# Kernel optimization log

Measured on AMD Instinct MI355X. Metric: run time of the kernel, lower is better.

The kernel has to match this reference:

```python
import jax, jax.numpy as jnp
import numpy as np

B, S, D_IN, D_OUT = 4, 2048, 1024, 1024

def setup_inputs() -> dict:
    key = jax.random.key(0)
    k1, k2, k3, k4 = jax.random.split(key, 4)
    x = jax.random.normal(k1, (B, S, D_IN), dtype=jnp.float32)
    # nn.Linear weights: [out, in]; y = x @ W.T
    scale = 1.0 / np.sqrt(D_IN)
    W_key = jax.random.uniform(k2, (D_OUT, D_IN), dtype=jnp.float32, minval=-scale, maxval=scale)
    W_query = jax.random.uniform(k3, (D_OUT, D_IN), dtype=jnp.float32, minval=-scale, maxval=scale)
    W_value = jax.random.uniform(k4, (D_OUT, D_IN), dtype=jnp.float32, minval=-scale, maxval=scale)
    return {"x": x, "W_key": W_key, "W_query": W_query, "W_value": W_value}

def reference(x, W_key, W_query, W_value):
    # x: [B, S, D_IN]; W_*: [D_OUT, D_IN]
    keys = jnp.einsum('bsd,od->bso', x, W_key)
    queries = jnp.einsum('bsd,od->bso', x, W_query)
    values = jnp.einsum('bsd,od->bso', x, W_value)
    # attn_scores: [B, S, S]
    scores = jnp.einsum('bqo,bko->bqk', queries, keys)
    inv_sqrt_d = 1.0 / jnp.sqrt(jnp.asarray(keys.shape[-1], dtype=scores.dtype))
    weights = jax.nn.softmax(scores * inv_sqrt_d, axis=-1)
    context = jnp.einsum('bqk,bko->bqo', weights, values)
    return context
```

## Files before the change

### kernel.cpp

```cpp
#include <hip/hip_runtime.h>

typedef unsigned short u16;
typedef __attribute__((ext_vector_type(4))) float f32x4;
typedef __attribute__((ext_vector_type(8))) short bf16x8;
typedef __attribute__((ext_vector_type(4))) u16 u16x4;
typedef __attribute__((ext_vector_type(8))) u16 u16x8;

__device__ __forceinline__ u16 f2bf(float f) {
    unsigned u = __float_as_uint(f);
    unsigned r = (u + 0x7FFFu + ((u >> 16) & 1u)) >> 16;
    return (u16)r;
}

__device__ __forceinline__ void gld16(const void* g, void* l) {
    __builtin_amdgcn_global_load_lds(
        (const __attribute__((address_space(1))) unsigned*)g,
        (__attribute__((address_space(3))) unsigned*)l,
        16, 0, 0);
}

__device__ __forceinline__ void xcd_map(int& bx, int& by, int& bz) {
    const int gx = gridDim.x, gxy = gridDim.x * gridDim.y;
    const int F = blockIdx.x + gx * (blockIdx.y + gridDim.y * blockIdx.z);
    const int cpx = (gxy * gridDim.z) >> 3;
    const int L = (F & 7) * cpx + (F >> 3);
    bz = L / gxy;
    const int r = L % gxy;
    by = r / gx;
    bx = r % gx;
}

__global__ __launch_bounds__(256) void prep_kernel(
    const float* __restrict__ x, const float* __restrict__ Wq,
    const float* __restrict__ Wk, const float* __restrict__ Wv,
    u16* __restrict__ xb, u16* __restrict__ wqk, u16* __restrict__ wvb,
    float* __restrict__ den) {
    const int NX = 2097152, NW = 262144;
    const int total = NX + 3 * NW + 2048;
    int i = blockIdx.x * blockDim.x + threadIdx.x;
    int stride = gridDim.x * blockDim.x;
    for (; i < total; i += stride) {
        const float* src; u16* dst; int j;
        if (i < NX)               { src = x;  dst = xb;            j = i; }
        else if (i < NX + NW)     { src = Wq; dst = wqk;           j = i - NX; }
        else if (i < NX + 2 * NW) { src = Wk; dst = wqk + 1048576; j = i - NX - NW; }
        else if (i < NX + 3 * NW) { src = Wv; dst = wvb;           j = i - NX - 2 * NW; }
        else { ((f32x4*)den)[i - NX - 3 * NW] = f32x4{0.f, 0.f, 0.f, 0.f}; continue; }
        f32x4 v = ((const f32x4*)src)[j];
        u16x4 o;
        o[0] = f2bf(v[0]); o[1] = f2bf(v[1]); o[2] = f2bf(v[2]); o[3] = f2bf(v[3]);
        ((u16x4*)dst)[j] = o;
    }
}

template <int EPI>
__global__ __launch_bounds__(512, 1) void gemm256(
    const u16* __restrict__ A, const u16* __restrict__ Bm, void* __restrict__ Cv,
    int K, int lda, int ldb, int ldc,
    long long sA, long long sB, long long sC, float scale,
    float* __restrict__ denom) {
    extern __shared__ char smem[];
    int bx, by, bz;
    xcd_map(bx, by, bz);
    const u16* Ab = A + (long long)bz * sA;
    const u16* Bb = Bm + (long long)bz * sB;

    const int tid  = threadIdx.x;
    const int lane = tid & 63;
    const int w    = tid >> 6;
    const int wm   = w >> 2;
    const int wn   = w & 3;
    const int rowBase = bx << 8;
    const int colBase = by << 8;
    const int NT = K >> 6;
    const int aRow = lane & 15;

    auto stage = [&](int tile, int h) {
        if (tile >= NT) return;
        const int db = tile & 1;
        const int kt = tile << 6;
        const u16* mat; int ldm, rb, halfRow; char* region;
        if (h == 0)      { mat = Ab; ldm = lda; rb = rowBase; halfRow = 0;   region = smem + db * 32768; }
        else if (h == 1) { mat = Bb; ldm = ldb; rb = colBase; halfRow = 0;   region = smem + 65536 + db * 32768; }
        else if (h == 2) { mat = Bb; ldm = ldb; rb = colBase; halfRow = 128; region = smem + 65536 + db * 32768; }
        else             { mat = Ab; ldm = lda; rb = rowBase; halfRow = 128; region = smem + db * 32768; }
#pragma unroll
        for (int i = 0; i < 2; i++) {
            int o    = ((i * 8 + w) << 10) + lane * 16;
            int r    = o >> 7;
            int slot = (o >> 4) & 7;
            const u16* g = mat + (size_t)(rb + halfRow + r) * ldm + kt +
                           ((slot ^ (r & 7)) << 3);
            gld16(g, region + halfRow * 128 + ((i * 8 + w) << 10));
        }
    };
    auto ldA = [&](int db, int row, int ks) -> bf16x8 {
        int byte = db * 32768 + row * 128 + ((((ks << 2) | (lane >> 4)) ^ (row & 7)) << 4);
        return *(const bf16x8*)(smem + byte);
    };
    auto ldB = [&](int db, int row, int ks) -> bf16x8 {
        int byte = 65536 + db * 32768 + row * 128 + ((((ks << 2) | (lane >> 4)) ^ (row & 7)) << 4);
        return *(const bf16x8*)(smem + byte);
    };

    f32x4 acc[8][4] = {};
    bf16x8 aF[4][2], b0[2][2], b1[2][2];

    stage(0, 0); stage(0, 3); stage(0, 1); stage(0, 2);
    stage(1, 1); stage(1, 2);
    __builtin_amdgcn_sched_barrier(0);
    asm volatile("s_waitcnt vmcnt(4)" ::: "memory");
    __builtin_amdgcn_sched_barrier(0);
    __builtin_amdgcn_s_barrier();

    for (int t = 0; t < NT; ++t) {
        const int db = t & 1;
#pragma unroll
        for (int m = 0; m < 4; m++)
#pragma unroll
            for (int ks = 0; ks < 2; ks++)
                aF[m][ks] = ldA(db, wm * 128 + m * 16 + aRow, ks);
#pragma unroll
        for (int n = 0; n < 2; n++)
#pragma unroll
            for (int ks = 0; ks < 2; ks++)
                b0[n][ks] = ldB(db, wn * 64 + n * 16 + aRow, ks);
        stage(t + 1, 0);
        __builtin_amdgcn_s_barrier();
        asm volatile("s_waitcnt lgkmcnt(0)" ::: "memory");
        __builtin_amdgcn_sched_barrier(0);
        __builtin_amdgcn_s_setprio(1);
#pragma unroll
        for (int ks = 0; ks < 2; ks++)
#pragma unroll
            for (int m = 0; m < 4; m++)
#pragma unroll
                for (int n = 0; n < 2; n++)
                    acc[m][n] = __builtin_amdgcn_mfma_f32_16x16x32_bf16(
                        aF[m][ks], b0[n][ks], acc[m][n], 0, 0, 0);
        __builtin_amdgcn_s_setprio(0);
#pragma unroll
        for (int n = 0; n < 2; n++)
#pragma unroll
            for (int ks = 0; ks < 2; ks++)
                b1[n][ks] = ldB(db, wn * 64 + (n + 2) * 16 + aRow, ks);
        stage(t + 1, 3);
        __builtin_amdgcn_s_barrier();
        asm volatile("s_waitcnt lgkmcnt(0)" ::: "memory");
        __builtin_amdgcn_sched_barrier(0);
        __builtin_amdgcn_s_setprio(1);
#pragma unroll
        for (int ks = 0; ks < 2; ks++)
#pragma unroll
            for (int m = 0; m < 4; m++)
#pragma unroll
                for (int n = 0; n < 2; n++)
                    acc[m][n + 2] = __builtin_amdgcn_mfma_f32_16x16x32_bf16(
                        aF[m][ks], b1[n][ks], acc[m][n + 2], 0, 0, 0);
        __builtin_amdgcn_s_setprio(0);
#pragma unroll
        for (int m = 0; m < 4; m++)
#pragma unroll
            for (int ks = 0; ks < 2; ks++)
                aF[m][ks] = ldA(db, wm * 128 + (m + 4) * 16 + aRow, ks);
        __builtin_amdgcn_s_barrier();
        asm volatile("s_waitcnt lgkmcnt(0)" ::: "memory");
        __builtin_amdgcn_sched_barrier(0);
        __builtin_amdgcn_s_setprio(1);
#pragma unroll
        for (int ks = 0; ks < 2; ks++)
#pragma unroll
            for (int m = 0; m < 4; m++)
#pragma unroll
                for (int n = 0; n < 2; n++)
                    acc[m + 4][n + 2] = __builtin_amdgcn_mfma_f32_16x16x32_bf16(
                        aF[m][ks], b1[n][ks], acc[m + 4][n + 2], 0, 0, 0);
        __builtin_amdgcn_s_setprio(0);
        stage(t + 2, 1);
        stage(t + 2, 2);
        __builtin_amdgcn_sched_barrier(0);
        if (t + 2 < NT) { asm volatile("s_waitcnt vmcnt(4)" ::: "memory"); }
        else            { asm volatile("s_waitcnt vmcnt(0)" ::: "memory"); }
        __builtin_amdgcn_sched_barrier(0);
        __builtin_amdgcn_s_barrier();
        __builtin_amdgcn_s_setprio(1);
#pragma unroll
        for (int ks = 0; ks < 2; ks++)
#pragma unroll
            for (int m = 0; m < 4; m++)
#pragma unroll
                for (int n = 0; n < 2; n++)
                    acc[m + 4][n] = __builtin_amdgcn_mfma_f32_16x16x32_bf16(
                        aF[m][ks], b0[n][ks], acc[m + 4][n], 0, 0, 0);
        __builtin_amdgcn_s_setprio(0);
    }

    const int row0 = rowBase + wm * 128 + ((lane >> 4) << 2);
    const int col0 = colBase + wn * 64 + (lane & 15);
    long long cb = (long long)bz * sC;
    if (EPI == 0) {
#pragma unroll
        for (int m = 0; m < 8; m++)
#pragma unroll
            for (int n = 0; n < 4; n++) {
                f32x4 v = acc[m][n];
#pragma unroll
                for (int j = 0; j < 4; j++) {
                    size_t idx = (size_t)(row0 + m * 16 + j) * ldc + (col0 + n * 16);
                    ((u16*)Cv)[cb + idx] = f2bf(v[j] * scale);
                }
            }
    } else {
        float* dz = denom + (long long)bz * 2048;
#pragma unroll
        for (int m = 0; m < 8; m++) {
#pragma unroll
            for (int j = 0; j < 4; j++) {
                const int row = row0 + m * 16 + j;
                float rs = 0.f;
#pragma unroll
                for (int n = 0; n < 4; n++) {
                    float e = __expf(fminf(acc[m][n][j] * scale, 60.f));
                    rs += e;
                    ((u16*)Cv)[cb + (size_t)row * ldc + (col0 + n * 16)] = f2bf(e);
                }
#pragma unroll
                for (int off = 1; off < 16; off <<= 1) rs += __shfl_xor(rs, off);
                if ((lane & 15) == 0) atomicAdd(&dz[row], rs);
            }
        }
    }
}

template <int EPI>
__global__ __launch_bounds__(512, 1) void gemm256n128(
    const u16* __restrict__ A, const u16* __restrict__ Bm, void* __restrict__ Cv,
    int K, int lda, int ldb, int ldc,
    long long sA, long long sB, long long sC, float scale,
    const float* __restrict__ denom) {
    extern __shared__ char smem[];
    int bx, by, bz;
    xcd_map(bx, by, bz);
    const u16* Ab = A + (long long)bz * sA;
    const u16* Bb = Bm + (long long)bz * sB;

    const int tid  = threadIdx.x;
    const int lane = tid & 63;
    const int w    = tid >> 6;
    const int wm   = w >> 1;
    const int wn   = w & 1;
    const int rowBase = bx << 8;
    const int colBase = by << 7;
    const int NT = K >> 6;
    const int aRow = lane & 15;

    auto stage = [&](int tile, int h) {
        if (tile >= NT) return;
        const int db = tile & 1;
        const int kt = tile << 6;
        if (h == 0 || h == 3) {
            const int halfRow = (h == 0) ? 0 : 128;
            char* region = smem + db * 32768;
#pragma unroll
            for (int i = 0; i < 2; i++) {
                int o    = i * 8192 + tid * 16;
                int r    = o >> 7;
                int slot = (o >> 4) & 7;
                const u16* g = Ab + (size_t)(rowBase + halfRow + r) * lda + kt +
                               ((slot ^ (r & 7)) << 3);
                gld16(g, region + halfRow * 128 + i * 8192 + (w << 10));
            }
        } else {
            const int halfRow = (h == 1) ? 0 : 64;
            char* region = smem + 65536 + db * 16384;
            int o    = tid * 16;
            int r    = o >> 7;
            int slot = (o >> 4) & 7;
            const u16* g = Bb + (size_t)(colBase + halfRow + r) * ldb + kt +
                           ((slot ^ (r & 7)) << 3);
            gld16(g, region + halfRow * 128 + (w << 10));
        }
    };
    auto ldA = [&](int db, int row, int ks) -> bf16x8 {
        int byte = db * 32768 + row * 128 + ((((ks << 2) | (lane >> 4)) ^ (row & 7)) << 4);
        return *(const bf16x8*)(smem + byte);
    };
    auto ldB = [&](int db, int row, int ks) -> bf16x8 {
        int byte = 65536 + db * 16384 + row * 128 + ((((ks << 2) | (lane >> 4)) ^ (row & 7)) << 4);
        return *(const bf16x8*)(smem + byte);
    };

    f32x4 acc[4][4] = {};
    bf16x8 aF[2][2], b0[2][2], b1[2][2];

    stage(0, 0); stage(0, 3); stage(0, 1); stage(0, 2);
    stage(1, 1); stage(1, 2);
    __builtin_amdgcn_sched_barrier(0);
    asm volatile("s_waitcnt vmcnt(2)" ::: "memory");
    __builtin_amdgcn_sched_barrier(0);
    __builtin_amdgcn_s_barrier();

    for (int t = 0; t < NT; ++t) {
        const int db = t & 1;
#pragma unroll
        for (int m = 0; m < 2; m++)
#pragma unroll
            for (int ks = 0; ks < 2; ks++)
                aF[m][ks] = ldA(db, wm * 64 + m * 16 + aRow, ks);
#pragma unroll
        for (int n = 0; n < 2; n++)
#pragma unroll
            for (int ks = 0; ks < 2; ks++)
                b0[n][ks] = ldB(db, wn * 64 + n * 16 + aRow, ks);
        stage(t + 1, 0);
        __builtin_amdgcn_s_barrier();
        asm volatile("s_waitcnt lgkmcnt(0)" ::: "memory");
        __builtin_amdgcn_sched_barrier(0);
        __builtin_amdgcn_s_setprio(1);
#pragma unroll
        for (int ks = 0; ks < 2; ks++)
#pragma unroll
            for (int m = 0; m < 2; m++)
#pragma unroll
                for (int n = 0; n < 2; n++)
                    acc[m][n] = __builtin_amdgcn_mfma_f32_16x16x32_bf16(
                        aF[m][ks], b0[n][ks], acc[m][n], 0, 0, 0);
        __builtin_amdgcn_s_setprio(0);
#pragma unroll
        for (int n = 0; n < 2; n++)
#pragma unroll
            for (int ks = 0; ks < 2; ks++)
                b1[n][ks] = ldB(db, wn * 64 + (n + 2) * 16 + aRow, ks);
        stage(t + 1, 3);
        __builtin_amdgcn_s_barrier();
        asm volatile("s_waitcnt lgkmcnt(0)" ::: "memory");
        __builtin_amdgcn_sched_barrier(0);
        __builtin_amdgcn_s_setprio(1);
#pragma unroll
        for (int ks = 0; ks < 2; ks++)
#pragma unroll
            for (int m = 0; m < 2; m++)
#pragma unroll
                for (int n = 0; n < 2; n++)
                    acc[m][n + 2] = __builtin_amdgcn_mfma_f32_16x16x32_bf16(
                        aF[m][ks], b1[n][ks], acc[m][n + 2], 0, 0, 0);
        __builtin_amdgcn_s_setprio(0);
#pragma unroll
        for (int m = 0; m < 2; m++)
#pragma unroll
            for (int ks = 0; ks < 2; ks++)
                aF[m][ks] = ldA(db, wm * 64 + (m + 2) * 16 + aRow, ks);
        __builtin_amdgcn_s_barrier();
        asm volatile("s_waitcnt lgkmcnt(0)" ::: "memory");
        __builtin_amdgcn_sched_barrier(0);
        __builtin_amdgcn_s_setprio(1);
#pragma unroll
        for (int ks = 0; ks < 2; ks++)
#pragma unroll
            for (int m = 0; m < 2; m++)
#pragma unroll
                for (int n = 0; n < 2; n++)
                    acc[m + 2][n + 2] = __builtin_amdgcn_mfma_f32_16x16x32_bf16(
                        aF[m][ks], b1[n][ks], acc[m + 2][n + 2], 0, 0, 0);
        __builtin_amdgcn_s_setprio(0);
        stage(t + 2, 1);
        stage(t + 2, 2);
        __builtin_amdgcn_sched_barrier(0);
        if (t + 2 < NT) { asm volatile("s_waitcnt vmcnt(2)" ::: "memory"); }
        else            { asm volatile("s_waitcnt vmcnt(0)" ::: "memory"); }
        __builtin_amdgcn_sched_barrier(0);
        __builtin_amdgcn_s_barrier();
        __builtin_amdgcn_s_setprio(1);
#pragma unroll
        for (int ks = 0; ks < 2; ks++)
#pragma unroll
            for (int m = 0; m < 2; m++)
#pragma unroll
                for (int n = 0; n < 2; n++)
                    acc[m + 2][n] = __builtin_amdgcn_mfma_f32_16x16x32_bf16(
                        aF[m][ks], b0[n][ks], acc[m + 2][n], 0, 0, 0);
        __builtin_amdgcn_s_setprio(0);
    }

    const int row0 = rowBase + wm * 64 + ((lane >> 4) << 2);
    const int col0 = colBase + wn * 64 + (lane & 15);
    long long cb = (long long)bz * sC;
    if (EPI == 0) {
#pragma unroll
        for (int m = 0; m < 4; m++)
#pragma unroll
            for (int n = 0; n < 4; n++) {
                f32x4 v = acc[m][n];
#pragma unroll
                for (int j = 0; j < 4; j++) {
                    size_t idx = (size_t)(row0 + m * 16 + j) * ldc + (col0 + n * 16);
                    ((u16*)Cv)[cb + idx] = f2bf(v[j] * scale);
                }
            }
    } else {
        const float* dz = denom + (long long)bz * 2048;
        float inv[4][4];
#pragma unroll
        for (int m = 0; m < 4; m++)
#pragma unroll
            for (int j = 0; j < 4; j++)
                inv[m][j] = 1.0f / dz[row0 + m * 16 + j];
#pragma unroll
        for (int m = 0; m < 4; m++)
#pragma unroll
            for (int n = 0; n < 4; n++) {
                f32x4 v = acc[m][n];
#pragma unroll
                for (int j = 0; j < 4; j++) {
                    size_t idx = (size_t)(row0 + m * 16 + j) * ldc + (col0 + n * 16);
                    ((float*)Cv)[cb + idx] = v[j] * inv[m][j];
                }
            }
    }
}

extern "C" void kernel_launch(void* const* d_in, const int* in_sizes, int n_in,
                              void* d_out, int out_size, void* d_ws, size_t ws_size,
                              hipStream_t stream) {
    const float* x  = (const float*)d_in[0];
    const float* Wk = (const float*)d_in[1];
    const float* Wq = (const float*)d_in[2];
    const float* Wv = (const float*)d_in[3];
    float* out = (float*)d_out;
    char* ws = (char*)d_ws;
    const size_t MB = 1u << 20;

    u16* xb    = (u16*)(ws);
    u16* Wqk   = (u16*)(ws + 16 * MB);
    u16* Wvb   = (u16*)(ws + 20 * MB);
    float* den = (float*)(ws + 24 * MB);
    u16* QK    = (u16*)(ws + 64 * MB);
    u16* VT    = (u16*)(ws + 96 * MB);
    u16* Pb    = (u16*)(ws + 112 * MB);

    const long long SS = 2048LL * 2048;

    hipFuncSetAttribute((const void*)gemm256<0>, hipFuncAttributeMaxDynamicSharedMemorySize, 131072);
    hipFuncSetAttribute((const void*)gemm256<2>, hipFuncAttributeMaxDynamicSharedMemorySize, 131072);
    hipFuncSetAttribute((const void*)gemm256n128<0>, hipFuncAttributeMaxDynamicSharedMemorySize, 98304);
    hipFuncSetAttribute((const void*)gemm256n128<3>, hipFuncAttributeMaxDynamicSharedMemorySize, 98304);

    prep_kernel<<<2048, 256, 0, stream>>>(x, Wq, Wk, Wv, xb, Wqk, Wvb, den);

    gemm256<0><<<dim3(32, 8, 1), 512, 131072, stream>>>(
        xb, Wqk, QK, 1024, 1024, 1024, 2048, 0, 0, 0, 1.0f, nullptr);
    gemm256n128<0><<<dim3(4, 64, 1), 512, 98304, stream>>>(
        Wvb, xb, VT, 1024, 1024, 1024, 8192, 0, 0, 0, 1.0f, nullptr);
    gemm256<2><<<dim3(8, 8, 4), 512, 131072, stream>>>(
        QK, QK + 1024, Pb, 1024, 2048, 2048, 2048, SS, SS, SS, 0.03125f, den);
    gemm256n128<3><<<dim3(8, 8, 4), 512, 98304, stream>>>(
        Pb, VT, out, 2048, 2048, 8192, 1024, SS, 2048LL, 2048LL * 1024, 1.0f, den);
}
```

Baseline: 146.3 us.

## Fold Wq and Wk into a single Wq^T·Wk matrix to replace K projection

Rewrites the scores as x·(Wq^T Wk)·x^T. A small 1024x1024 product G is computed from transposed bf16 weights, and Q' = x·G is computed. The scores GEMM then uses Q' against x directly, so the separate K projection disappears. In its place come a weight transpose in the prep kernel and a small weight-only GEMM, with a different rounding path because G is stored in bf16.

```diff
diff --git a/kernel.cpp b/kernel.cpp
--- a/kernel.cpp
+++ b/kernel.cpp
@@ -33,23 +33,51 @@
 __global__ __launch_bounds__(256) void prep_kernel(
     const float* __restrict__ x, const float* __restrict__ Wq,
     const float* __restrict__ Wk, const float* __restrict__ Wv,
-    u16* __restrict__ xb, u16* __restrict__ wqk, u16* __restrict__ wvb,
-    float* __restrict__ den) {
-    const int NX = 2097152, NW = 262144;
-    const int total = NX + 3 * NW + 2048;
-    int i = blockIdx.x * blockDim.x + threadIdx.x;
-    int stride = gridDim.x * blockDim.x;
-    for (; i < total; i += stride) {
-        const float* src; u16* dst; int j;
-        if (i < NX)               { src = x;  dst = xb;            j = i; }
-        else if (i < NX + NW)     { src = Wq; dst = wqk;           j = i - NX; }
-        else if (i < NX + 2 * NW) { src = Wk; dst = wqk + 1048576; j = i - NX - NW; }
-        else if (i < NX + 3 * NW) { src = Wv; dst = wvb;           j = i - NX - 2 * NW; }
-        else { ((f32x4*)den)[i - NX - 3 * NW] = f32x4{0.f, 0.f, 0.f, 0.f}; continue; }
-        f32x4 v = ((const f32x4*)src)[j];
-        u16x4 o;
-        o[0] = f2bf(v[0]); o[1] = f2bf(v[1]); o[2] = f2bf(v[2]); o[3] = f2bf(v[3]);
-        ((u16x4*)dst)[j] = o;
+    u16* __restrict__ xb, u16* __restrict__ wqt, u16* __restrict__ wkt,
+    u16* __restrict__ wvb, float* __restrict__ den) {
+    const int NX = 2097152, NWV = 262144;
+    const int tid = threadIdx.x;
+    if (blockIdx.x < 1536) {
+        const int total = NX + NWV + 2048;
+        int i = blockIdx.x * 256 + tid;
+        int stride = 1536 * 256;
+        for (; i < total; i += stride) {
+            const float* src; u16* dst; int j;
+            if (i < NX)            { src = x;  dst = xb;  j = i; }
+            else if (i < NX + NWV) { src = Wv; dst = wvb; j = i - NX; }
+            else { ((f32x4*)den)[i - NX - NWV] = f32x4{0.f, 0.f, 0.f, 0.f}; continue; }
+            f32x4 v = ((const f32x4*)src)[j];
+            u16x4 o;
+            o[0] = f2bf(v[0]); o[1] = f2bf(v[1]); o[2] = f2bf(v[2]); o[3] = f2bf(v[3]);
+            ((u16x4*)dst)[j] = o;
+        }
+    } else {
+        __shared__ u16 tile[64][65];
+        const int t2  = blockIdx.x - 1536;
+        const int mat = t2 >> 8;
+        const int t16 = t2 & 255;
+        const int o0  = (t16 >> 4) << 6;
+        const int i0  = (t16 & 15) << 6;
+        const float* src = mat ? Wk : Wq;
+        u16* dst = mat ? wkt : wqt;
+#pragma unroll
+        for (int p = 0; p < 4; p++) {
+            int idx = p * 256 + tid;
+            int r = idx >> 4, c4 = (idx & 15) << 2;
+            f32x4 v = *(const f32x4*)(src + (size_t)(o0 + r) * 1024 + i0 + c4);
+#pragma unroll
+            for (int q = 0; q < 4; q++) tile[r][c4 + q] = f2bf(v[q]);
+        }
+        __syncthreads();
+#pragma unroll
+        for (int p = 0; p < 4; p++) {
+            int idx = p * 256 + tid;
+            int ii = idx >> 4, oc4 = (idx & 15) << 2;
+            u16x4 o4;
+#pragma unroll
+            for (int q = 0; q < 4; q++) o4[q] = tile[oc4 + q][ii];
+            *(u16x4*)(dst + (size_t)(i0 + ii) * 1024 + o0 + oc4) = o4;
+        }
     }
 }
 
@@ -431,28 +459,32 @@
     const size_t MB = 1u << 20;
 
     u16* xb    = (u16*)(ws);
-    u16* Wqk   = (u16*)(ws + 16 * MB);
+    u16* WqT   = (u16*)(ws + 16 * MB);
+    u16* WkT   = (u16*)(ws + 18 * MB);
     u16* Wvb   = (u16*)(ws + 20 * MB);
+    u16* GT    = (u16*)(ws + 22 * MB);
     float* den = (float*)(ws + 24 * MB);
-    u16* QK    = (u16*)(ws + 64 * MB);
+    u16* Qp    = (u16*)(ws + 32 * MB);
     u16* VT    = (u16*)(ws + 96 * MB);
     u16* Pb    = (u16*)(ws + 112 * MB);
 
+    const long long SB = 2048LL * 1024;
     const long long SS = 2048LL * 2048;
 
-    hipFuncSetAttribute((const void*)gemm256<0>, hipFuncAttributeMaxDynamicSharedMemorySize, 131072);
     hipFuncSetAttribute((const void*)gemm256<2>, hipFuncAttributeMaxDynamicSharedMemorySize, 131072);
     hipFuncSetAttribute((const void*)gemm256n128<0>, hipFuncAttributeMaxDynamicSharedMemorySize, 98304);
     hipFuncSetAttribute((const void*)gemm256n128<3>, hipFuncAttributeMaxDynamicSharedMemorySize, 98304);
 
-    prep_kernel<<<2048, 256, 0, stream>>>(x, Wq, Wk, Wv, xb, Wqk, Wvb, den);
-
-    gemm256<0><<<dim3(32, 8, 1), 512, 131072, stream>>>(
-        xb, Wqk, QK, 1024, 1024, 1024, 2048, 0, 0, 0, 1.0f, nullptr);
+    prep_kernel<<<2048, 256, 0, stream>>>(x, Wq, Wk, Wv, xb, WqT, WkT, Wvb, den);
+
+    gemm256n128<0><<<dim3(4, 8, 1), 512, 98304, stream>>>(
+        WkT, WqT, GT, 1024, 1024, 1024, 1024, 0, 0, 0, 1.0f, nullptr);
     gemm256n128<0><<<dim3(4, 64, 1), 512, 98304, stream>>>(
         Wvb, xb, VT, 1024, 1024, 1024, 8192, 0, 0, 0, 1.0f, nullptr);
+    gemm256n128<0><<<dim3(32, 8, 1), 512, 98304, stream>>>(
+        xb, GT, Qp, 1024, 1024, 1024, 1024, 0, 0, 0, 1.0f, nullptr);
     gemm256<2><<<dim3(8, 8, 4), 512, 131072, stream>>>(
-        QK, QK + 1024, Pb, 1024, 2048, 2048, 2048, SS, SS, SS, 0.03125f, den);
+        Qp, xb, Pb, 1024, 1024, 1024, 2048, SB, SB, SS, 0.03125f, den);
     gemm256n128<3><<<dim3(8, 8, 4), 512, 98304, stream>>>(
         Pb, VT, out, 2048, 2048, 8192, 1024, SS, 2048LL, 2048LL * 1024, 1.0f, den);
 }
```

New measurement: 152.7 us. 4.4% more time.
